# Performance work log

Measured on AMD Instinct MI355X. Metric: run time of the kernel, lower is better.

## Reference

```python
import jax, jax.numpy as jnp
from jax import lax
import numpy as np

B, N, C = 16, 4096, 81          # batch, rois, classes (incl. background)
VARIANCES = np.array([0.1, 0.1, 0.2, 0.2], dtype=np.float32)
MAX_TOTAL = 200                  # max_total_size (= per-class cap here)
K = 200                          # per-class candidates kept before NMS
SCORE_TH = 0.5
IOU_TH = 0.5                     # tf combined NMS default
EPS = 1e-8


def setup_inputs() -> dict:
    key = jax.random.key(0)
    k1, k2, k3, k4 = jax.random.split(key, 4)
    yx = jax.random.uniform(k1, (B, N, 2)) * 0.8
    hw = 0.05 + jax.random.uniform(k2, (B, N, 2)) * 0.15
    roi_bboxes = jnp.concatenate([yx, yx + hw], axis=-1)          # [B,N,4] y1x1y2x2 in [0,1]
    pred_deltas = jax.random.normal(k3, (B, N, C * 4)) * 0.5      # [B,N,C*4]
    logits = jax.random.normal(k4, (B, N, C)) * 3.0
    pred_label_probs = jax.nn.softmax(logits, axis=-1)            # [B,N,C]
    return {"roi_bboxes": roi_bboxes, "pred_deltas": pred_deltas,
            "pred_label_probs": pred_label_probs}


def delta_to_bbox(anchors, deltas):
    # anchors [...,4] y1,x1,y2,x2 ; deltas [...,4] dy,dx,dh,dw
    ah = anchors[..., 2] - anchors[..., 0]
    aw = anchors[..., 3] - anchors[..., 1]
    acy = anchors[..., 0] + 0.5 * ah
    acx = anchors[..., 1] + 0.5 * aw
    bh = jnp.exp(deltas[..., 2]) * ah
    bw = jnp.exp(deltas[..., 3]) * aw
    bcy = deltas[..., 0] * ah + acy
    bcx = deltas[..., 1] * aw + acx
    y1 = bcy - 0.5 * bh
    x1 = bcx - 0.5 * bw
    return jnp.stack([y1, x1, y1 + bh, x1 + bw], axis=-1)


def pairwise_iou(boxes):  # [K,4] -> [K,K]
    y1 = jnp.maximum(boxes[:, None, 0], boxes[None, :, 0])
    x1 = jnp.maximum(boxes[:, None, 1], boxes[None, :, 1])
    y2 = jnp.minimum(boxes[:, None, 2], boxes[None, :, 2])
    x2 = jnp.minimum(boxes[:, None, 3], boxes[None, :, 3])
    inter = jnp.maximum(y2 - y1, 0.0) * jnp.maximum(x2 - x1, 0.0)
    area = jnp.maximum(boxes[:, 2] - boxes[:, 0], 0.0) * jnp.maximum(boxes[:, 3] - boxes[:, 1], 0.0)
    union = area[:, None] + area[None, :] - inter
    return inter / (union + EPS)


def _nms_keep(boxes_k, scores_k):
    # boxes_k [K,4] sorted by score desc; greedy suppression mask
    ious = pairwise_iou(boxes_k)
    rng = jnp.arange(K)
    valid = scores_k > SCORE_TH

    def step(keep, i):
        sup = (ious[i] > IOU_TH) & (rng > i) & keep[i]
        return keep & ~sup, None

    keep, _ = lax.scan(step, valid, rng)
    return keep


def _per_class(boxes_c, scores_c):
    # boxes_c [N,4], scores_c [N] -> top-K candidates + NMS-kept scores
    sc, idx = lax.top_k(scores_c, K)
    bx = boxes_c[idx]                       # [K,4]
    keep = _nms_keep(bx, sc)
    return bx, jnp.where(keep, sc, 0.0)


def _per_image(boxes_b, scores_b):
    # boxes_b [N,C,4], scores_b [N,C]
    bx, sc = jax.vmap(_per_class, in_axes=(1, 1))(boxes_b, scores_b)  # [C,K,4],[C,K]
    top_sc, top_idx = lax.top_k(sc.reshape(-1), MAX_TOTAL)
    top_bx = bx.reshape(-1, 4)[top_idx]
    top_lbl = (top_idx // K).astype(jnp.float32)
    valid = top_sc > 0.0
    top_bx = jnp.clip(jnp.where(valid[:, None], top_bx, 0.0), 0.0, 1.0)  # clip_boxes=True
    return top_bx, jnp.where(valid, top_sc, 0.0), jnp.where(valid, top_lbl, 0.0)


def reference(roi_bboxes, pred_deltas, pred_label_probs):
    b, n, _ = roi_bboxes.shape
    c = pred_label_probs.shape[-1]
    deltas = pred_deltas.reshape(b, n, c, 4) * jnp.asarray(VARIANCES)
    pred_bboxes = delta_to_bbox(roi_bboxes[:, :, None, :], deltas)       # [B,N,C,4]
    bg = jnp.argmax(pred_label_probs, axis=-1) == 0                      # background mask
    scores = jnp.where(bg[..., None], 0.0, pred_label_probs)             # [B,N,C]
    final_bboxes, final_scores, final_labels = jax.vmap(_per_image)(pred_bboxes, scores)
    return final_bboxes, final_labels, final_scores
```

## Files before the change

kernel.cpp:

```cpp
#include <hip/hip_runtime.h>
#include <math.h>

#pragma clang fp contract(off)

constexpr int NB  = 16;
constexpr int NR  = 4096;
constexpr int NC  = 81;
constexpr int KK  = 200;
constexpr int CAP = 4096;
constexpr int SEGCAP = 1024;
constexpr int ROWS_PER_BLK = 64;
constexpr int GRID = NB * NR / ROWS_PER_BLK;
constexpr int TCHUNK = 256;
constexpr int NCHUNK = CAP / TCHUNK;
constexpr float SCORE_TH = 0.5f;
constexpr float IOU_TH   = 0.5f;
constexpr float EPSF     = 1e-8f;

struct Entry {
    float s;
    int   cls;
    int   aux;
    int   pad;
    float y1, x1, y2, x2;
};
static_assert(sizeof(Entry) == 32, "Entry must be 32B");

struct SK { float s; int key; };

__device__ __forceinline__ void decode_box(const float4& a, const float4& d,
                                           float& y1, float& x1, float& y2, float& x2) {
    float ah  = a.z - a.x;
    float aw  = a.w - a.y;
    float acy = a.x + 0.5f * ah;
    float acx = a.y + 0.5f * aw;
    float dy = d.x * 0.1f, dx = d.y * 0.1f;
    float dh = d.z * 0.2f, dw = d.w * 0.2f;
    float bh  = expf(dh) * ah;
    float bw  = expf(dw) * aw;
    float bcy = dy * ah + acy;
    float bcx = dx * aw + acx;
    y1 = bcy - 0.5f * bh;
    x1 = bcx - 0.5f * bw;
    y2 = y1 + bh;
    x2 = x1 + bw;
}

__global__ void k_init(int* __restrict__ counts) {
    int i = blockIdx.x * blockDim.x + threadIdx.x;
    if (i < NB * NC + NB) counts[i] = 0;
}

__global__ void k_classify(const float* __restrict__ roi,
                           const float* __restrict__ deltas,
                           const float* __restrict__ probs,
                           int* __restrict__ counts,
                           Entry* __restrict__ cand) {
    __shared__ float lp[ROWS_PER_BLK * NC];
    const float4* src = (const float4*)(probs + (size_t)blockIdx.x * ROWS_PER_BLK * NC);
    float4* dst = (float4*)lp;
    for (int v = threadIdx.x; v < ROWS_PER_BLK * NC / 4; v += blockDim.x) dst[v] = src[v];
    __syncthreads();

    int g = threadIdx.x >> 2;
    int j = threadIdx.x & 3;
    const float* row = lp + g * NC;
    float m = -1.0f;
    int am = 127;
    for (int c = j; c < NC; c += 4) {
        float v = row[c];
        if (v > m) { m = v; am = c; }
    }
    for (int mask = 1; mask <= 2; mask <<= 1) {
        float om = __shfl_xor(m, mask);
        int   oi = __shfl_xor(am, mask);
        if (om > m || (om == m && oi < am)) { m = om; am = oi; }
    }
    if (j != 0) return;
    if (am == 0 || !(m > SCORE_TH)) return;

    int r = blockIdx.x * ROWS_PER_BLK + g;
    int b = r / NR;
    float4 a = ((const float4*)roi)[r];
    float4 d = *(const float4*)(deltas + ((size_t)r * NC + am) * 4);
    float y1, x1, y2, x2;
    decode_box(a, d, y1, x1, y2, x2);
    int slot = atomicAdd(&counts[b * NC + am], 1);
    if (slot < SEGCAP) {
        Entry* e = &cand[(size_t)(b * NC + am) * SEGCAP + slot];
        e->s = m; e->cls = am; e->aux = r % NR; e->pad = 0;
        e->y1 = y1; e->x1 = x1; e->y2 = y2; e->x2 = x2;
    }
}

__global__ void k_perclass(const int* __restrict__ counts,
                           const Entry* __restrict__ cand,
                           int* __restrict__ final_count,
                           Entry* __restrict__ fin,
                           SK* __restrict__ sk) {
    int b = blockIdx.x / NC, c = blockIdx.x % NC;
    if (c == 0) return;
    int Mc = counts[b * NC + c];
    if (Mc > SEGCAP) Mc = SEGCAP;
    if (Mc == 0) return;
    const Entry* seg = cand + (size_t)(b * NC + c) * SEGCAP;

    __shared__ float ls[SEGCAP], ly1[SEGCAP], lx1[SEGCAP], ly2[SEGCAP], lx2[SEGCAP];
    __shared__ int   lroi[SEGCAP];
    __shared__ float ss[KK], sy1[KK], sx1[KK], sy2[KK], sx2[KK], sar[KK];
    __shared__ unsigned long long sup[KK][4];
    __shared__ int   skeep[KK];
    __shared__ int   sbase;

    for (int i = threadIdx.x; i < Mc; i += blockDim.x) {
        Entry e = seg[i];
        ls[i] = e.s; lroi[i] = e.aux;
        ly1[i] = e.y1; lx1[i] = e.x1; ly2[i] = e.y2; lx2[i] = e.x2;
    }
    __syncthreads();

    for (int i = threadIdx.x; i < Mc; i += blockDim.x) {
        float si = ls[i]; int ri = lroi[i];
        int rank = 0;
        for (int j = 0; j < Mc; ++j) {
            float sj = ls[j]; int rj = lroi[j];
            rank += (int)((sj > si) | ((sj == si) & (rj < ri)));
        }
        if (rank < KK) {
            ss[rank] = si;
            sy1[rank] = ly1[i]; sx1[rank] = lx1[i];
            sy2[rank] = ly2[i]; sx2[rank] = lx2[i];
            sar[rank] = fmaxf(ly2[i] - ly1[i], 0.f) * fmaxf(lx2[i] - lx1[i], 0.f);
        }
    }
    __syncthreads();

    int L = Mc < KK ? Mc : KK;

    for (int idx = threadIdx.x; idx < L * 4; idx += blockDim.x) {
        int i = idx >> 2, w = idx & 3;
        int j0 = w * 64;
        unsigned long long bits = 0;
        int jend = j0 + 64 < L ? j0 + 64 : L;
        int jstart = j0 > i + 1 ? j0 : i + 1;
        if (jstart < jend) {
            float yi1 = sy1[i], xi1 = sx1[i], yi2 = sy2[i], xi2 = sx2[i], ai = sar[i];
            for (int j = jstart; j < jend; ++j) {
                float yy1 = fmaxf(yi1, sy1[j]), xx1 = fmaxf(xi1, sx1[j]);
                float yy2 = fminf(yi2, sy2[j]), xx2 = fminf(xi2, sx2[j]);
                float inter = fmaxf(yy2 - yy1, 0.f) * fmaxf(xx2 - xx1, 0.f);
                float uni = ai + sar[j] - inter;
                if (inter / (uni + EPSF) > IOU_TH) bits |= 1ull << (j - j0);
            }
        }
        sup[i][w] = bits;
    }
    __syncthreads();

    if (threadIdx.x < 64) {
        int lane = threadIdx.x;
        int kmask = 0;
        #pragma unroll
        for (int s = 0; s < 4; ++s) if (s * 64 + lane < L) kmask |= 1 << s;

        for (int i = 0; i < L; ++i) {
            int oi = i & 63, si = i >> 6;
            unsigned long long r0 = sup[i][0], r1 = sup[i][1];
            unsigned long long r2 = sup[i][2], r3 = sup[i][3];
            int keep_i = (__shfl(kmask, oi) >> si) & 1;
            if (keep_i) {
                int supb = (int)((r0 >> lane) & 1)
                         | ((int)((r1 >> lane) & 1) << 1)
                         | ((int)((r2 >> lane) & 1) << 2)
                         | ((int)((r3 >> lane) & 1) << 3);
                kmask &= ~supb;
            }
        }
        #pragma unroll
        for (int s = 0; s < 4; ++s) {
            int jj = s * 64 + lane;
            if (jj < L) skeep[jj] = (kmask >> s) & 1;
        }
    }
    __syncthreads();

    if (threadIdx.x == 0) {
        int tot = 0;
        for (int i = 0; i < L; ++i) tot += skeep[i];
        sbase = atomicAdd(&final_count[b], tot);
    }
    __syncthreads();
    int base = sbase;

    for (int i = threadIdx.x; i < L; i += blockDim.x) {
        if (skeep[i]) {
            int pos = 0;
            for (int j = 0; j < i; ++j) pos += skeep[j];
            int slot = base + pos;
            if (slot < CAP) {
                Entry* fo = &fin[(size_t)b * CAP + slot];
                fo->s = ss[i]; fo->cls = c; fo->aux = i; fo->pad = 0;
                fo->y1 = sy1[i]; fo->x1 = sx1[i]; fo->y2 = sy2[i]; fo->x2 = sx2[i];
                sk[(size_t)b * CAP + slot].s = ss[i];
                sk[(size_t)b * CAP + slot].key = c * KK + i;
            }
        }
    }
}

__global__ void k_topk(const int* __restrict__ final_count,
                       const Entry* __restrict__ fin,
                       const SK* __restrict__ sk,
                       float* __restrict__ out) {
    int b = blockIdx.x / NCHUNK, chunk = blockIdx.x % NCHUNK;
    int M = final_count[b];
    if (M > CAP) M = CAP;

    float* obox = out + (size_t)b * KK * 4;
    float* olbl = out + (size_t)NB * KK * 4 + (size_t)b * KK;
    float* osc  = out + (size_t)NB * KK * 5 + (size_t)b * KK;

    if (chunk == 0) {
        int Mi = M < KK ? M : KK;
        for (int i = Mi + (int)threadIdx.x; i < KK; i += blockDim.x) {
            obox[i * 4 + 0] = 0.f; obox[i * 4 + 1] = 0.f;
            obox[i * 4 + 2] = 0.f; obox[i * 4 + 3] = 0.f;
            olbl[i] = 0.f; osc[i] = 0.f;
        }
    }
    if (chunk * TCHUNK >= M) return;

    __shared__ SK sL[CAP];
    const float2* src = (const float2*)(sk + (size_t)b * CAP);
    float2* dstv = (float2*)sL;
    for (int i = threadIdx.x; i < M; i += blockDim.x) dstv[i] = src[i];
    __syncthreads();

    int e = chunk * TCHUNK + threadIdx.x;
    if (e >= M) return;
    float se = sL[e].s; int ke = sL[e].key;
    int rank = 0;
    const float4* p4 = (const float4*)sL;
    int npair = M >> 1;
    #pragma unroll 4
    for (int p = 0; p < npair; ++p) {
        float4 v = p4[p];
        int k0 = __float_as_int(v.y), k1 = __float_as_int(v.w);
        rank += (int)((v.x > se) | ((v.x == se) & (k0 < ke)));
        rank += (int)((v.z > se) | ((v.z == se) & (k1 < ke)));
    }
    if (M & 1) {
        float sj = sL[M - 1].s; int kj = sL[M - 1].key;
        rank += (int)((sj > se) | ((sj == se) & (kj < ke)));
    }
    if (rank < KK) {
        Entry en = fin[(size_t)b * CAP + e];
        obox[rank * 4 + 0] = fminf(fmaxf(en.y1, 0.f), 1.f);
        obox[rank * 4 + 1] = fminf(fmaxf(en.x1, 0.f), 1.f);
        obox[rank * 4 + 2] = fminf(fmaxf(en.y2, 0.f), 1.f);
        obox[rank * 4 + 3] = fminf(fmaxf(en.x2, 0.f), 1.f);
        olbl[rank] = (float)en.cls;
        osc[rank]  = en.s;
    }
}

extern "C" void kernel_launch(void* const* d_in, const int* in_sizes, int n_in,
                              void* d_out, int out_size, void* d_ws, size_t ws_size,
                              hipStream_t stream) {
    const float* roi    = (const float*)d_in[0];
    const float* deltas = (const float*)d_in[1];
    const float* probs  = (const float*)d_in[2];
    float* out = (float*)d_out;

    int* ws_i        = (int*)d_ws;
    int* counts      = ws_i;
    int* final_count = ws_i + NB * NC;
    Entry* cand = (Entry*)((char*)d_ws + 16384);
    Entry* fin  = cand + (size_t)NB * NC * SEGCAP;
    SK*    sk   = (SK*)(fin + (size_t)NB * CAP);

    k_init<<<(NB * NC + NB + 255) / 256, 256, 0, stream>>>(counts);
    k_classify<<<GRID, 256, 0, stream>>>(roi, deltas, probs, counts, cand);
    k_perclass<<<NB * NC, 256, 0, stream>>>(counts, cand, final_count, fin, sk);
    k_topk<<<NB * NCHUNK, 256, 0, stream>>>(final_count, fin, sk, out);
}
```

Before: 80.69 us.

## Replace per-class atomic buckets with block-compacted survivors scanned per class

The classify kernel now compacts surviving rows per block with a wave ballot and prefix sum, writing class, score/roi and box arrays in SoA form, and zeroes final_count itself so the init kernel launch disappears. Each per-class block scans all of its image's compacted survivors (4096 slots) to gather entries for its class into shared memory, then loads boxes only for the top-K ranks. The 32-byte Entry struct is dropped in favor of float4 boxes, with labels recovered from the sort key. This removes global atomics on per-class counters and one launch, at the cost of every class block rereading the whole image's class array.

```diff
diff --git a/kernel.cpp b/kernel.cpp
--- a/kernel.cpp
+++ b/kernel.cpp
@@ -8,23 +8,15 @@
 constexpr int NC  = 81;
 constexpr int KK  = 200;
 constexpr int CAP = 4096;
-constexpr int SEGCAP = 1024;
 constexpr int ROWS_PER_BLK = 64;
+constexpr int CHUNKS = NR / ROWS_PER_BLK;
 constexpr int GRID = NB * NR / ROWS_PER_BLK;
+constexpr int MAXC = 1024;
 constexpr int TCHUNK = 256;
 constexpr int NCHUNK = CAP / TCHUNK;
 constexpr float SCORE_TH = 0.5f;
 constexpr float IOU_TH   = 0.5f;
 constexpr float EPSF     = 1e-8f;
-
-struct Entry {
-    float s;
-    int   cls;
-    int   aux;
-    int   pad;
-    float y1, x1, y2, x2;
-};
-static_assert(sizeof(Entry) == 32, "Entry must be 32B");
 
 struct SK { float s; int key; };
 
@@ -46,24 +38,25 @@
     x2 = x1 + bw;
 }
 
-__global__ void k_init(int* __restrict__ counts) {
-    int i = blockIdx.x * blockDim.x + threadIdx.x;
-    if (i < NB * NC + NB) counts[i] = 0;
-}
-
 __global__ void k_classify(const float* __restrict__ roi,
                            const float* __restrict__ deltas,
                            const float* __restrict__ probs,
-                           int* __restrict__ counts,
-                           Entry* __restrict__ cand) {
+                           int* __restrict__ blk_cnt,
+                           int* __restrict__ final_count,
+                           int* __restrict__ scls,
+                           float2* __restrict__ ssr,
+                           float4* __restrict__ sbox) {
     __shared__ float lp[ROWS_PER_BLK * NC];
-    const float4* src = (const float4*)(probs + (size_t)blockIdx.x * ROWS_PER_BLK * NC);
+    __shared__ int wcnt[4], wbase[4];
+    const int bid = blockIdx.x, tid = threadIdx.x;
+
+    const float4* src = (const float4*)(probs + (size_t)bid * ROWS_PER_BLK * NC);
     float4* dst = (float4*)lp;
-    for (int v = threadIdx.x; v < ROWS_PER_BLK * NC / 4; v += blockDim.x) dst[v] = src[v];
-    __syncthreads();
-
-    int g = threadIdx.x >> 2;
-    int j = threadIdx.x & 3;
+    for (int v = tid; v < ROWS_PER_BLK * NC / 4; v += 256) dst[v] = src[v];
+    __syncthreads();
+
+    int g = tid >> 2;
+    int j = tid & 3;
     const float* row = lp + g * NC;
     float m = -1.0f;
     int am = 127;
@@ -76,68 +69,93 @@
         int   oi = __shfl_xor(am, mask);
         if (om > m || (om == m && oi < am)) { m = om; am = oi; }
     }
-    if (j != 0) return;
-    if (am == 0 || !(m > SCORE_TH)) return;
-
-    int r = blockIdx.x * ROWS_PER_BLK + g;
-    int b = r / NR;
-    float4 a = ((const float4*)roi)[r];
-    float4 d = *(const float4*)(deltas + ((size_t)r * NC + am) * 4);
-    float y1, x1, y2, x2;
-    decode_box(a, d, y1, x1, y2, x2);
-    int slot = atomicAdd(&counts[b * NC + am], 1);
-    if (slot < SEGCAP) {
-        Entry* e = &cand[(size_t)(b * NC + am) * SEGCAP + slot];
-        e->s = m; e->cls = am; e->aux = r % NR; e->pad = 0;
-        e->y1 = y1; e->x1 = x1; e->y2 = y2; e->x2 = x2;
-    }
-}
-
-__global__ void k_perclass(const int* __restrict__ counts,
-                           const Entry* __restrict__ cand,
+
+    bool pred = (j == 0) && (am != 0) && (m > SCORE_TH);
+    unsigned long long bal = __ballot(pred);
+    int lane = tid & 63, w = tid >> 6;
+    if (lane == 0) wcnt[w] = __popcll(bal);
+    __syncthreads();
+    if (tid == 0) {
+        int run = 0;
+        for (int i = 0; i < 4; ++i) { wbase[i] = run; run += wcnt[i]; }
+        blk_cnt[bid] = run;
+        if ((bid & (CHUNKS - 1)) == 0) final_count[bid / CHUNKS] = 0;
+    }
+    __syncthreads();
+
+    if (pred) {
+        int pos = wbase[w] + __popcll(bal & ((1ull << lane) - 1ull));
+        int r = bid * ROWS_PER_BLK + g;
+        float4 a = ((const float4*)roi)[r];
+        float4 d = *(const float4*)(deltas + ((size_t)r * NC + am) * 4);
+        float y1, x1, y2, x2;
+        decode_box(a, d, y1, x1, y2, x2);
+        int idx = bid * ROWS_PER_BLK + pos;
+        scls[idx] = am;
+        ssr[idx]  = make_float2(m, (float)(r & (NR - 1)));
+        sbox[idx] = make_float4(y1, x1, y2, x2);
+    }
+}
+
+__global__ void k_perclass(const int* __restrict__ blk_cnt,
+                           const int* __restrict__ scls,
+                           const float2* __restrict__ ssr,
+                           const float4* __restrict__ sbox,
                            int* __restrict__ final_count,
-                           Entry* __restrict__ fin,
+                           float4* __restrict__ fbox,
                            SK* __restrict__ sk) {
+    __shared__ int ccnt[CHUNKS];
+    __shared__ int lcnt;
+    __shared__ float ls[MAXC], lroi[MAXC];
+    __shared__ unsigned short lidx[MAXC];
+    __shared__ float ss[KK], sy1[KK], sx1[KK], sy2[KK], sx2[KK], sar[KK];
+    __shared__ unsigned long long sup[KK][4];
+    __shared__ int skeep[KK];
+    __shared__ int sbase;
+
     int b = blockIdx.x / NC, c = blockIdx.x % NC;
     if (c == 0) return;
-    int Mc = counts[b * NC + c];
-    if (Mc > SEGCAP) Mc = SEGCAP;
+    const int tid = threadIdx.x;
+
+    if (tid < CHUNKS) ccnt[tid] = blk_cnt[b * CHUNKS + tid];
+    if (tid == 0) lcnt = 0;
+    __syncthreads();
+
+    const int* sc = scls + (size_t)b * NR;
+    const float2* sr = ssr + (size_t)b * NR;
+    for (int sidx = tid; sidx < NR; sidx += 256) {
+        int chunk = sidx >> 6, s = sidx & 63;
+        if (s < ccnt[chunk] && sc[sidx] == c) {
+            int p = atomicAdd(&lcnt, 1);
+            if (p < MAXC) {
+                float2 v = sr[sidx];
+                ls[p] = v.x; lroi[p] = v.y; lidx[p] = (unsigned short)sidx;
+            }
+        }
+    }
+    __syncthreads();
+    int Mc = lcnt; if (Mc > MAXC) Mc = MAXC;
     if (Mc == 0) return;
-    const Entry* seg = cand + (size_t)(b * NC + c) * SEGCAP;
-
-    __shared__ float ls[SEGCAP], ly1[SEGCAP], lx1[SEGCAP], ly2[SEGCAP], lx2[SEGCAP];
-    __shared__ int   lroi[SEGCAP];
-    __shared__ float ss[KK], sy1[KK], sx1[KK], sy2[KK], sx2[KK], sar[KK];
-    __shared__ unsigned long long sup[KK][4];
-    __shared__ int   skeep[KK];
-    __shared__ int   sbase;
-
-    for (int i = threadIdx.x; i < Mc; i += blockDim.x) {
-        Entry e = seg[i];
-        ls[i] = e.s; lroi[i] = e.aux;
-        ly1[i] = e.y1; lx1[i] = e.x1; ly2[i] = e.y2; lx2[i] = e.x2;
-    }
-    __syncthreads();
-
-    for (int i = threadIdx.x; i < Mc; i += blockDim.x) {
-        float si = ls[i]; int ri = lroi[i];
+
+    for (int i = tid; i < Mc; i += 256) {
+        float si = ls[i], ri = lroi[i];
         int rank = 0;
-        for (int j = 0; j < Mc; ++j) {
-            float sj = ls[j]; int rj = lroi[j];
+        for (int jj = 0; jj < Mc; ++jj) {
+            float sj = ls[jj], rj = lroi[jj];
             rank += (int)((sj > si) | ((sj == si) & (rj < ri)));
         }
         if (rank < KK) {
+            float4 bx = sbox[(size_t)b * NR + lidx[i]];
             ss[rank] = si;
-            sy1[rank] = ly1[i]; sx1[rank] = lx1[i];
-            sy2[rank] = ly2[i]; sx2[rank] = lx2[i];
-            sar[rank] = fmaxf(ly2[i] - ly1[i], 0.f) * fmaxf(lx2[i] - lx1[i], 0.f);
+            sy1[rank] = bx.x; sx1[rank] = bx.y; sy2[rank] = bx.z; sx2[rank] = bx.w;
+            sar[rank] = fmaxf(bx.z - bx.x, 0.f) * fmaxf(bx.w - bx.y, 0.f);
         }
     }
     __syncthreads();
 
     int L = Mc < KK ? Mc : KK;
 
-    for (int idx = threadIdx.x; idx < L * 4; idx += blockDim.x) {
+    for (int idx = tid; idx < L * 4; idx += 256) {
         int i = idx >> 2, w = idx & 3;
         int j0 = w * 64;
         unsigned long long bits = 0;
@@ -157,12 +175,11 @@
     }
     __syncthreads();
 
-    if (threadIdx.x < 64) {
-        int lane = threadIdx.x;
+    if (tid < 64) {
+        int lane = tid;
         int kmask = 0;
         #pragma unroll
         for (int s = 0; s < 4; ++s) if (s * 64 + lane < L) kmask |= 1 << s;
-
         for (int i = 0; i < L; ++i) {
             int oi = i & 63, si = i >> 6;
             unsigned long long r0 = sup[i][0], r1 = sup[i][1];
@@ -184,7 +201,7 @@
     }
     __syncthreads();
 
-    if (threadIdx.x == 0) {
+    if (tid == 0) {
         int tot = 0;
         for (int i = 0; i < L; ++i) tot += skeep[i];
         sbase = atomicAdd(&final_count[b], tot);
@@ -192,15 +209,13 @@
     __syncthreads();
     int base = sbase;
 
-    for (int i = threadIdx.x; i < L; i += blockDim.x) {
+    for (int i = tid; i < L; i += 256) {
         if (skeep[i]) {
             int pos = 0;
             for (int j = 0; j < i; ++j) pos += skeep[j];
             int slot = base + pos;
             if (slot < CAP) {
-                Entry* fo = &fin[(size_t)b * CAP + slot];
-                fo->s = ss[i]; fo->cls = c; fo->aux = i; fo->pad = 0;
-                fo->y1 = sy1[i]; fo->x1 = sx1[i]; fo->y2 = sy2[i]; fo->x2 = sx2[i];
+                fbox[(size_t)b * CAP + slot] = make_float4(sy1[i], sx1[i], sy2[i], sx2[i]);
                 sk[(size_t)b * CAP + slot].s = ss[i];
                 sk[(size_t)b * CAP + slot].key = c * KK + i;
             }
@@ -209,7 +224,7 @@
 }
 
 __global__ void k_topk(const int* __restrict__ final_count,
-                       const Entry* __restrict__ fin,
+                       const float4* __restrict__ fbox,
                        const SK* __restrict__ sk,
                        float* __restrict__ out) {
     int b = blockIdx.x / NCHUNK, chunk = blockIdx.x % NCHUNK;
@@ -254,13 +269,13 @@
         rank += (int)((sj > se) | ((sj == se) & (kj < ke)));
     }
     if (rank < KK) {
-        Entry en = fin[(size_t)b * CAP + e];
-        obox[rank * 4 + 0] = fminf(fmaxf(en.y1, 0.f), 1.f);
-        obox[rank * 4 + 1] = fminf(fmaxf(en.x1, 0.f), 1.f);
-        obox[rank * 4 + 2] = fminf(fmaxf(en.y2, 0.f), 1.f);
-        obox[rank * 4 + 3] = fminf(fmaxf(en.x2, 0.f), 1.f);
-        olbl[rank] = (float)en.cls;
-        osc[rank]  = en.s;
+        float4 bx = fbox[(size_t)b * CAP + e];
+        obox[rank * 4 + 0] = fminf(fmaxf(bx.x, 0.f), 1.f);
+        obox[rank * 4 + 1] = fminf(fmaxf(bx.y, 0.f), 1.f);
+        obox[rank * 4 + 2] = fminf(fmaxf(bx.z, 0.f), 1.f);
+        obox[rank * 4 + 3] = fminf(fmaxf(bx.w, 0.f), 1.f);
+        olbl[rank] = (float)(ke / KK);
+        osc[rank]  = se;
     }
 }
 
@@ -272,15 +287,18 @@
     const float* probs  = (const float*)d_in[2];
     float* out = (float*)d_out;
 
-    int* ws_i        = (int*)d_ws;
-    int* counts      = ws_i;
-    int* final_count = ws_i + NB * NC;
-    Entry* cand = (Entry*)((char*)d_ws + 16384);
-    Entry* fin  = cand + (size_t)NB * NC * SEGCAP;
-    SK*    sk   = (SK*)(fin + (size_t)NB * CAP);
-
-    k_init<<<(NB * NC + NB + 255) / 256, 256, 0, stream>>>(counts);
-    k_classify<<<GRID, 256, 0, stream>>>(roi, deltas, probs, counts, cand);
-    k_perclass<<<NB * NC, 256, 0, stream>>>(counts, cand, final_count, fin, sk);
-    k_topk<<<NB * NCHUNK, 256, 0, stream>>>(final_count, fin, sk, out);
-}
+    char* base = (char*)d_ws;
+    int*    blk_cnt     = (int*)base;
+    int*    final_count = (int*)(base + 4096);
+    int*    scls        = (int*)(base + 8192);
+    float2* ssr         = (float2*)(base + 8192 + 262144);
+    float4* sbox        = (float4*)(base + 8192 + 262144 + 524288);
+    float4* fbox        = (float4*)(base + 8192 + 262144 + 524288 + 1048576);
+    SK*     sk          = (SK*)(base + 8192 + 262144 + 524288 + 1048576 + 1048576);
+
+    k_classify<<<GRID, 256, 0, stream>>>(roi, deltas, probs, blk_cnt, final_count,
+                                         scls, ssr, sbox);
+    k_perclass<<<NB * NC, 256, 0, stream>>>(blk_cnt, scls, ssr, sbox,
+                                            final_count, fbox, sk);
+    k_topk<<<NB * NCHUNK, 256, 0, stream>>>(final_count, fbox, sk, out);
+}
```

After: 72.37 us. 1.11x faster.
